# Optimization experiments

Hardware: AMD Instinct MI355X
Metric: run time of the kernel (lower is better)

The kernel has to match this reference:

```python
import jax, jax.numpy as jnp
import numpy as np

I_DIM = 50000
D_DIM = 128
N_EDGES = 800000
N_NODES = I_DIM + 1


def setup_inputs() -> dict:
    key = jax.random.key(0)
    k1, k2, k3, k4 = jax.random.split(key, 4)
    # edge[:,0] must be sorted for the original bincount+repeat normalization to be valid
    src = jnp.sort(jax.random.randint(k1, (N_EDGES,), 0, N_NODES))
    dst = jax.random.randint(k2, (N_EDGES,), 0, N_NODES)
    edge = jnp.stack([src, dst], axis=1).astype(jnp.int64)
    # GlorotNormal-style init for the embedding table and dense layers
    emb_mat = jax.random.normal(k3, (N_NODES, D_DIM), dtype=jnp.float32) * np.sqrt(2.0 / (N_NODES + D_DIM))
    kA, kB = jax.random.split(k4)
    W_scale = jax.random.normal(kA, (D_DIM, D_DIM), dtype=jnp.float32) * np.sqrt(2.0 / (2 * D_DIM))
    b_scale = jnp.zeros((D_DIM,), dtype=jnp.float32)
    W_att = jax.random.normal(kB, (2 * D_DIM, 1), dtype=jnp.float32) * np.sqrt(2.0 / (2 * D_DIM + 1))
    b_att = jnp.zeros((1,), dtype=jnp.float32)
    return {"edge": edge, "emb_mat": emb_mat, "W_scale": W_scale,
            "b_scale": b_scale, "W_att": W_att, "b_att": b_att}


def reference(edge, emb_mat, W_scale, b_scale, W_att, b_att):
    E = edge.shape[0]
    src = edge[:, 0]
    dst = edge[:, 1]
    # gather both endpoints, project: [E, 2, d]
    edge_emb = jnp.einsum('epd,df->epf', emb_mat[edge], W_scale) + b_scale
    edge_emb = edge_emb.reshape(E, -1)                       # [E, 2d]
    att = edge_emb @ W_att + b_att                           # [E, 1]
    att = jnp.where(att >= 0, att, 0.2 * att)                # LeakyReLU(0.2)
    att = jnp.squeeze(att, axis=-1)                          # [E]
    scores = jnp.exp(att - 1.0)
    score_sum = jax.ops.segment_sum(scores, src, num_segments=N_NODES)
    score_norm = scores / score_sum[src]                     # segment softmax
    item_scaled = emb_mat @ W_scale + b_scale                # [N, d]
    msgs = score_norm[:, None] * item_scaled[dst]            # [E, d]
    agg = jax.ops.segment_sum(msgs, src, num_segments=N_NODES)
    return jax.nn.sigmoid(agg)                               # [N, d]
```

## Files before the change

### kernel.cpp

```cpp
#include <hip/hip_runtime.h>
#include <math.h>


#define NN 50001
#define DD 128
#define NE 800000
#define GEMM_BLOCKS 782
#define EDGE_BLOCKS 3125
#define TR_BLOCKS 64

typedef __attribute__((ext_vector_type(8))) short short8;
typedef __attribute__((ext_vector_type(4))) float floatx4;

__device__ __forceinline__ unsigned short f2bf(float f) {
    unsigned u = __builtin_bit_cast(unsigned, f);
    u += 0x7fffu + ((u >> 16) & 1u);
    return (unsigned short)(u >> 16);
}
__device__ __forceinline__ float bflo(unsigned u) {
    return __builtin_bit_cast(float, u << 16);
}
__device__ __forceinline__ float bfhi(unsigned u) {
    return __builtin_bit_cast(float, u & 0xffff0000u);
}
__device__ __forceinline__ float score(float att) {
    att = att >= 0.f ? att : 0.2f * att;
    return __expf(att - 1.f);
}

__global__ void __launch_bounds__(256) k_pre(const float* __restrict__ W,
        const int* __restrict__ edge, unsigned short* __restrict__ WT,
        int* __restrict__ row_ptr) {
    if (blockIdx.x < TR_BLOCKS) {
        int j = blockIdx.x * 2 + (threadIdx.x >> 7);
        int k = threadIdx.x & 127;
        WT[j * DD + k] = f2bf(W[k * DD + j]);
        return;
    }
    int e = (blockIdx.x - TR_BLOCKS) * 256 + threadIdx.x;
    if (e >= NE) return;
    int s = edge[2 * e];
    if (e == 0) {
        for (int n = 0; n <= s; n++) row_ptr[n] = 0;
    } else {
        int p = edge[2 * (e - 1)];
        for (int n = p + 1; n <= s; n++) row_ptr[n] = e;
    }
    if (e == NE - 1) {
        for (int n = s + 1; n <= NN; n++) row_ptr[n] = NE;
    }
}

__global__ void __launch_bounds__(256) k_gemm(const float* __restrict__ emb,
        const unsigned short* __restrict__ WT, const float* __restrict__ b_scale,
        const float* __restrict__ W_att, unsigned short* __restrict__ item,
        float* __restrict__ a_src, float* __restrict__ a_dst,
        const float* __restrict__ b_att) {
    int wave = blockIdx.x * 4 + (threadIdx.x >> 6);
    int lane = threadIdx.x & 63;
    int base = wave * 16;
    if (base >= NN) return;
    int m = lane & 15, q = lane >> 4;
    int node = base + m;
    bool valid = node < NN;

    int row = valid ? node : NN - 1;
    const float* bp = emb + (long)row * DD + q * 8;
    short8 b[4];
    #pragma unroll
    for (int ks = 0; ks < 4; ks++) {
        float4 f0 = *(const float4*)(bp + ks * 32);
        float4 f1 = *(const float4*)(bp + ks * 32 + 4);
        b[ks][0] = (short)f2bf(f0.x); b[ks][1] = (short)f2bf(f0.y);
        b[ks][2] = (short)f2bf(f0.z); b[ks][3] = (short)f2bf(f0.w);
        b[ks][4] = (short)f2bf(f1.x); b[ks][5] = (short)f2bf(f1.y);
        b[ks][6] = (short)f2bf(f1.z); b[ks][7] = (short)f2bf(f1.w);
    }

    float p_src = 0.f, p_dst = 0.f;

    #pragma unroll
    for (int ft = 0; ft < 8; ft++) {
        floatx4 acc = {0.f, 0.f, 0.f, 0.f};
        const unsigned short* wrow = WT + (ft * 16 + m) * DD;
        #pragma unroll
        for (int ks = 0; ks < 4; ks++) {
            short8 a = *(const short8*)(wrow + ks * 32 + q * 8);
            acc = __builtin_amdgcn_mfma_f32_16x16x32_bf16(a, b[ks], acc, 0, 0, 0);
        }
        int fo = ft * 16 + q * 4;
        float4 bs = *(const float4*)(b_scale + fo);
        float4 ws = *(const float4*)(W_att + fo);
        float4 wd = *(const float4*)(W_att + DD + fo);
        float v0 = acc[0] + bs.x, v1 = acc[1] + bs.y;
        float v2 = acc[2] + bs.z, v3 = acc[3] + bs.w;
        if (valid) {
            uint2 pk;
            pk.x = (unsigned)f2bf(v0) | ((unsigned)f2bf(v1) << 16);
            pk.y = (unsigned)f2bf(v2) | ((unsigned)f2bf(v3) << 16);
            *(uint2*)(item + (long)node * DD + fo) = pk;
        }
        p_src += v0 * ws.x + v1 * ws.y + v2 * ws.z + v3 * ws.w;
        p_dst += v0 * wd.x + v1 * wd.y + v2 * wd.z + v3 * wd.w;
    }
    p_src += __shfl_xor(p_src, 16, 64); p_src += __shfl_xor(p_src, 32, 64);
    p_dst += __shfl_xor(p_dst, 16, 64); p_dst += __shfl_xor(p_dst, 32, 64);
    if (q == 0 && valid) { a_src[node] = p_src + b_att[0]; a_dst[node] = p_dst; }
}

#define ACC8(S, U) \
    acc[0] += (S) * bflo((U).x); acc[1] += (S) * bfhi((U).x); \
    acc[2] += (S) * bflo((U).y); acc[3] += (S) * bfhi((U).y); \
    acc[4] += (S) * bflo((U).z); acc[5] += (S) * bfhi((U).z); \
    acc[6] += (S) * bflo((U).w); acc[7] += (S) * bfhi((U).w);

__global__ void __launch_bounds__(256) k_agg(const int* __restrict__ edge,
        const int* __restrict__ row_ptr, const unsigned short* __restrict__ item,
        const float* __restrict__ a_src, const float* __restrict__ a_dst,
        float* __restrict__ out) {
    int n = blockIdx.x * 16 + (threadIdx.x >> 4);
    int t = threadIdx.x & 15;
    if (n >= NN) return;

    int start = row_ptr[n];
    int len = row_ptr[n + 1] - start;
    float* op = out + (long)n * DD + t * 8;

    if (len <= 0) {
        float4 h = make_float4(0.5f, 0.5f, 0.5f, 0.5f);
        *(float4*)op = h;
        *(float4*)(op + 4) = h;
        return;
    }

    float asrc = a_src[n];
    const int* dp = edge + 2 * start + 1;
    const unsigned short* ip = item + t * 8;

    float acc[8] = {0.f, 0.f, 0.f, 0.f, 0.f, 0.f, 0.f, 0.f};
    float ssum = 0.f;

    for (int j = 0; j < len; j += 16) {
        int jj = j + t;
        int idx = jj < len ? jj : len - 1;
        int d = dp[2 * idx];
        float x = a_dst[d];
        float s = (jj < len) ? score(asrc + x) : 0.f;
        ssum += s;

        int cnt = len - j;
        if (cnt > 16) cnt = 16;
        int kk = 0;
        for (; kk + 4 <= cnt; kk += 4) {
            int d0 = __shfl(d, kk, 16),     d1 = __shfl(d, kk + 1, 16);
            int d2 = __shfl(d, kk + 2, 16), d3 = __shfl(d, kk + 3, 16);
            float s0 = __shfl(s, kk, 16),     s1 = __shfl(s, kk + 1, 16);
            float s2 = __shfl(s, kk + 2, 16), s3 = __shfl(s, kk + 3, 16);
            uint4 u0 = *(const uint4*)(ip + (long)d0 * DD);
            uint4 u1 = *(const uint4*)(ip + (long)d1 * DD);
            uint4 u2 = *(const uint4*)(ip + (long)d2 * DD);
            uint4 u3 = *(const uint4*)(ip + (long)d3 * DD);
            ACC8(s0, u0);
            ACC8(s1, u1);
            ACC8(s2, u2);
            ACC8(s3, u3);
        }
        for (; kk < cnt; kk++) {
            int d0 = __shfl(d, kk, 16);
            float s0 = __shfl(s, kk, 16);
            uint4 u0 = *(const uint4*)(ip + (long)d0 * DD);
            ACC8(s0, u0);
        }
    }

    ssum += __shfl_xor(ssum, 1, 16);
    ssum += __shfl_xor(ssum, 2, 16);
    ssum += __shfl_xor(ssum, 4, 16);
    ssum += __shfl_xor(ssum, 8, 16);
    float inv = 1.f / ssum;

    float4 o0, o1;
    o0.x = 1.f / (1.f + __expf(-acc[0] * inv));
    o0.y = 1.f / (1.f + __expf(-acc[1] * inv));
    o0.z = 1.f / (1.f + __expf(-acc[2] * inv));
    o0.w = 1.f / (1.f + __expf(-acc[3] * inv));
    o1.x = 1.f / (1.f + __expf(-acc[4] * inv));
    o1.y = 1.f / (1.f + __expf(-acc[5] * inv));
    o1.z = 1.f / (1.f + __expf(-acc[6] * inv));
    o1.w = 1.f / (1.f + __expf(-acc[7] * inv));
    *(float4*)op = o0;
    *(float4*)(op + 4) = o1;
}

extern "C" void kernel_launch(void* const* d_in, const int* in_sizes, int n_in,
                              void* d_out, int out_size, void* d_ws, size_t ws_size,
                              hipStream_t stream) {
    const int*   edge    = (const int*)d_in[0];
    const float* emb     = (const float*)d_in[1];
    const float* W_scale = (const float*)d_in[2];
    const float* b_scale = (const float*)d_in[3];
    const float* W_att   = (const float*)d_in[4];
    const float* b_att   = (const float*)d_in[5];
    float* out = (float*)d_out;

    char* ws = (char*)d_ws;
    int*            row_ptr = (int*)(ws);
    float*          a_src   = (float*)(ws + 200832);
    float*          a_dst   = (float*)(ws + 401024);
    unsigned short* item    = (unsigned short*)(ws + 601216);
    unsigned short* WT      = (unsigned short*)(ws + 13401472);

    int node_blocks = (NN + 15) / 16;

    k_pre  <<<TR_BLOCKS + EDGE_BLOCKS, 256, 0, stream>>>(W_scale, edge, WT, row_ptr);
    k_gemm <<<GEMM_BLOCKS,             256, 0, stream>>>(emb, WT, b_scale, W_att,
                                                         item, a_src, a_dst, b_att);
    k_agg  <<<node_blocks,             256, 0, stream>>>(edge, row_ptr, item,
                                                         a_src, a_dst, out);
}
```

Before: 143.1 us.

## Apply W_scale after aggregation and fold attention weights into projected vectors

Uses linearity to reorder the work: the attention logits come from emb dotted with W_scale·W_att vectors computed once, and aggregation gathers bf16 raw embeddings, with the W_scale GEMM applied afterwards to the normalized aggregates in a new output kernel. Because the softmax weights sum to one per node, the bias can be added after the projection. This removes the pre-aggregation GEMM from the attention path, but adds a fourth kernel and an intermediate bf16 aggregate round trip, and the rounding points change slightly.

```diff
diff --git a/kernel.cpp b/kernel.cpp
--- a/kernel.cpp
+++ b/kernel.cpp
@@ -5,8 +5,9 @@
 #define NN 50001
 #define DD 128
 #define NE 800000
-#define GEMM_BLOCKS 782
 #define EDGE_BLOCKS 3125
+#define ATT_BLOCKS 3126
+#define OUT_BLOCKS 782
 #define TR_BLOCKS 64
 
 typedef __attribute__((ext_vector_type(8))) short short8;
@@ -29,7 +30,10 @@
 }
 
 __global__ void __launch_bounds__(256) k_pre(const float* __restrict__ W,
-        const int* __restrict__ edge, unsigned short* __restrict__ WT,
+        const float* __restrict__ W_att, const float* __restrict__ b_scale,
+        const float* __restrict__ b_att, const int* __restrict__ edge,
+        unsigned short* __restrict__ WT, float* __restrict__ u_src,
+        float* __restrict__ u_dst, float* __restrict__ cb,
         int* __restrict__ row_ptr) {
     if (blockIdx.x < TR_BLOCKS) {
         int j = blockIdx.x * 2 + (threadIdx.x >> 7);
@@ -37,7 +41,28 @@
         WT[j * DD + k] = f2bf(W[k * DD + j]);
         return;
     }
-    int e = (blockIdx.x - TR_BLOCKS) * 256 + threadIdx.x;
+    if (blockIdx.x == TR_BLOCKS) {
+        int k = threadIdx.x;
+        if (k < DD) {
+            float us = 0.f, ud = 0.f;
+            for (int j = 0; j < DD; j++) {
+                float w = W[k * DD + j];
+                us += w * W_att[j];
+                ud += w * W_att[DD + j];
+            }
+            u_src[k] = us; u_dst[k] = ud;
+        } else if (k == DD) {
+            float c = b_att[0];
+            for (int j = 0; j < DD; j++) c += b_scale[j] * W_att[j];
+            cb[0] = c;
+        } else if (k == DD + 1) {
+            float c = 0.f;
+            for (int j = 0; j < DD; j++) c += b_scale[j] * W_att[DD + j];
+            cb[1] = c;
+        }
+        return;
+    }
+    int e = (blockIdx.x - TR_BLOCKS - 1) * 256 + threadIdx.x;
     if (e >= NE) return;
     int s = edge[2 * e];
     if (e == 0) {
@@ -51,61 +76,39 @@
     }
 }
 
-__global__ void __launch_bounds__(256) k_gemm(const float* __restrict__ emb,
-        const unsigned short* __restrict__ WT, const float* __restrict__ b_scale,
-        const float* __restrict__ W_att, unsigned short* __restrict__ item,
-        float* __restrict__ a_src, float* __restrict__ a_dst,
-        const float* __restrict__ b_att) {
-    int wave = blockIdx.x * 4 + (threadIdx.x >> 6);
-    int lane = threadIdx.x & 63;
-    int base = wave * 16;
-    if (base >= NN) return;
-    int m = lane & 15, q = lane >> 4;
-    int node = base + m;
-    bool valid = node < NN;
-
-    int row = valid ? node : NN - 1;
-    const float* bp = emb + (long)row * DD + q * 8;
-    short8 b[4];
-    #pragma unroll
-    for (int ks = 0; ks < 4; ks++) {
-        float4 f0 = *(const float4*)(bp + ks * 32);
-        float4 f1 = *(const float4*)(bp + ks * 32 + 4);
-        b[ks][0] = (short)f2bf(f0.x); b[ks][1] = (short)f2bf(f0.y);
-        b[ks][2] = (short)f2bf(f0.z); b[ks][3] = (short)f2bf(f0.w);
-        b[ks][4] = (short)f2bf(f1.x); b[ks][5] = (short)f2bf(f1.y);
-        b[ks][6] = (short)f2bf(f1.z); b[ks][7] = (short)f2bf(f1.w);
-    }
-
-    float p_src = 0.f, p_dst = 0.f;
-
-    #pragma unroll
-    for (int ft = 0; ft < 8; ft++) {
-        floatx4 acc = {0.f, 0.f, 0.f, 0.f};
-        const unsigned short* wrow = WT + (ft * 16 + m) * DD;
-        #pragma unroll
-        for (int ks = 0; ks < 4; ks++) {
-            short8 a = *(const short8*)(wrow + ks * 32 + q * 8);
-            acc = __builtin_amdgcn_mfma_f32_16x16x32_bf16(a, b[ks], acc, 0, 0, 0);
-        }
-        int fo = ft * 16 + q * 4;
-        float4 bs = *(const float4*)(b_scale + fo);
-        float4 ws = *(const float4*)(W_att + fo);
-        float4 wd = *(const float4*)(W_att + DD + fo);
-        float v0 = acc[0] + bs.x, v1 = acc[1] + bs.y;
-        float v2 = acc[2] + bs.z, v3 = acc[3] + bs.w;
-        if (valid) {
-            uint2 pk;
-            pk.x = (unsigned)f2bf(v0) | ((unsigned)f2bf(v1) << 16);
-            pk.y = (unsigned)f2bf(v2) | ((unsigned)f2bf(v3) << 16);
-            *(uint2*)(item + (long)node * DD + fo) = pk;
-        }
-        p_src += v0 * ws.x + v1 * ws.y + v2 * ws.z + v3 * ws.w;
-        p_dst += v0 * wd.x + v1 * wd.y + v2 * wd.z + v3 * wd.w;
-    }
-    p_src += __shfl_xor(p_src, 16, 64); p_src += __shfl_xor(p_src, 32, 64);
-    p_dst += __shfl_xor(p_dst, 16, 64); p_dst += __shfl_xor(p_dst, 32, 64);
-    if (q == 0 && valid) { a_src[node] = p_src + b_att[0]; a_dst[node] = p_dst; }
+__global__ void __launch_bounds__(256) k_att(const float* __restrict__ emb,
+        const float* __restrict__ u_src, const float* __restrict__ u_dst,
+        const float* __restrict__ cb, unsigned short* __restrict__ emb_bf,
+        float* __restrict__ a_src, float* __restrict__ a_dst) {
+    int n = blockIdx.x * 16 + (threadIdx.x >> 4);
+    int t = threadIdx.x & 15;
+    if (n >= NN) return;
+
+    const float* ep = emb + (long)n * DD + t * 8;
+    float4 e0 = *(const float4*)(ep);
+    float4 e1 = *(const float4*)(ep + 4);
+    float4 us0 = *(const float4*)(u_src + t * 8);
+    float4 us1 = *(const float4*)(u_src + t * 8 + 4);
+    float4 ud0 = *(const float4*)(u_dst + t * 8);
+    float4 ud1 = *(const float4*)(u_dst + t * 8 + 4);
+
+    float ps = e0.x * us0.x + e0.y * us0.y + e0.z * us0.z + e0.w * us0.w
+             + e1.x * us1.x + e1.y * us1.y + e1.z * us1.z + e1.w * us1.w;
+    float pd = e0.x * ud0.x + e0.y * ud0.y + e0.z * ud0.z + e0.w * ud0.w
+             + e1.x * ud1.x + e1.y * ud1.y + e1.z * ud1.z + e1.w * ud1.w;
+
+    uint4 pk;
+    pk.x = (unsigned)f2bf(e0.x) | ((unsigned)f2bf(e0.y) << 16);
+    pk.y = (unsigned)f2bf(e0.z) | ((unsigned)f2bf(e0.w) << 16);
+    pk.z = (unsigned)f2bf(e1.x) | ((unsigned)f2bf(e1.y) << 16);
+    pk.w = (unsigned)f2bf(e1.z) | ((unsigned)f2bf(e1.w) << 16);
+    *(uint4*)(emb_bf + (long)n * DD + t * 8) = pk;
+
+    ps += __shfl_xor(ps, 1, 16); ps += __shfl_xor(ps, 2, 16);
+    ps += __shfl_xor(ps, 4, 16); ps += __shfl_xor(ps, 8, 16);
+    pd += __shfl_xor(pd, 1, 16); pd += __shfl_xor(pd, 2, 16);
+    pd += __shfl_xor(pd, 4, 16); pd += __shfl_xor(pd, 8, 16);
+    if (t == 0) { a_src[n] = ps + cb[0]; a_dst[n] = pd + cb[1]; }
 }
 
 #define ACC8(S, U) \
@@ -115,27 +118,26 @@
     acc[6] += (S) * bflo((U).w); acc[7] += (S) * bfhi((U).w);
 
 __global__ void __launch_bounds__(256) k_agg(const int* __restrict__ edge,
-        const int* __restrict__ row_ptr, const unsigned short* __restrict__ item,
+        const int* __restrict__ row_ptr, const unsigned short* __restrict__ emb_bf,
         const float* __restrict__ a_src, const float* __restrict__ a_dst,
-        float* __restrict__ out) {
+        unsigned short* __restrict__ aggN) {
     int n = blockIdx.x * 16 + (threadIdx.x >> 4);
     int t = threadIdx.x & 15;
     if (n >= NN) return;
 
     int start = row_ptr[n];
     int len = row_ptr[n + 1] - start;
-    float* op = out + (long)n * DD + t * 8;
+    unsigned short* op = aggN + (long)n * DD + t * 8;
 
     if (len <= 0) {
-        float4 h = make_float4(0.5f, 0.5f, 0.5f, 0.5f);
-        *(float4*)op = h;
-        *(float4*)(op + 4) = h;
+        uint4 z = make_uint4(0u, 0u, 0u, 0u);
+        *(uint4*)op = z;
         return;
     }
 
     float asrc = a_src[n];
     const int* dp = edge + 2 * start + 1;
-    const unsigned short* ip = item + t * 8;
+    const unsigned short* ip = emb_bf + t * 8;
 
     float acc[8] = {0.f, 0.f, 0.f, 0.f, 0.f, 0.f, 0.f, 0.f};
     float ssum = 0.f;
@@ -179,17 +181,57 @@
     ssum += __shfl_xor(ssum, 8, 16);
     float inv = 1.f / ssum;
 
-    float4 o0, o1;
-    o0.x = 1.f / (1.f + __expf(-acc[0] * inv));
-    o0.y = 1.f / (1.f + __expf(-acc[1] * inv));
-    o0.z = 1.f / (1.f + __expf(-acc[2] * inv));
-    o0.w = 1.f / (1.f + __expf(-acc[3] * inv));
-    o1.x = 1.f / (1.f + __expf(-acc[4] * inv));
-    o1.y = 1.f / (1.f + __expf(-acc[5] * inv));
-    o1.z = 1.f / (1.f + __expf(-acc[6] * inv));
-    o1.w = 1.f / (1.f + __expf(-acc[7] * inv));
-    *(float4*)op = o0;
-    *(float4*)(op + 4) = o1;
+    uint4 pk;
+    pk.x = (unsigned)f2bf(acc[0] * inv) | ((unsigned)f2bf(acc[1] * inv) << 16);
+    pk.y = (unsigned)f2bf(acc[2] * inv) | ((unsigned)f2bf(acc[3] * inv) << 16);
+    pk.z = (unsigned)f2bf(acc[4] * inv) | ((unsigned)f2bf(acc[5] * inv) << 16);
+    pk.w = (unsigned)f2bf(acc[6] * inv) | ((unsigned)f2bf(acc[7] * inv) << 16);
+    *(uint4*)op = pk;
+}
+
+__global__ void __launch_bounds__(256) k_out(const unsigned short* __restrict__ aggN,
+        const unsigned short* __restrict__ WT, const float* __restrict__ b_scale,
+        const int* __restrict__ row_ptr, float* __restrict__ out) {
+    int wave = blockIdx.x * 4 + (threadIdx.x >> 6);
+    int lane = threadIdx.x & 63;
+    int base = wave * 16;
+    if (base >= NN) return;
+    int m = lane & 15, q = lane >> 4;
+    int node = base + m;
+    bool valid = node < NN;
+    int row = valid ? node : NN - 1;
+    int len = row_ptr[row + 1] - row_ptr[row];
+
+    const unsigned short* bp = aggN + (long)row * DD + q * 8;
+    short8 b[4];
+    #pragma unroll
+    for (int ks = 0; ks < 4; ks++)
+        b[ks] = *(const short8*)(bp + ks * 32);
+
+    #pragma unroll
+    for (int ft = 0; ft < 8; ft++) {
+        floatx4 acc = {0.f, 0.f, 0.f, 0.f};
+        const unsigned short* wrow = WT + (ft * 16 + m) * DD + q * 8;
+        #pragma unroll
+        for (int ks = 0; ks < 4; ks++) {
+            short8 a = *(const short8*)(wrow + ks * 32);
+            acc = __builtin_amdgcn_mfma_f32_16x16x32_bf16(a, b[ks], acc, 0, 0, 0);
+        }
+        if (valid) {
+            int fo = ft * 16 + q * 4;
+            float4 bs = *(const float4*)(b_scale + fo);
+            float4 o;
+            if (len > 0) {
+                o.x = 1.f / (1.f + __expf(-(acc[0] + bs.x)));
+                o.y = 1.f / (1.f + __expf(-(acc[1] + bs.y)));
+                o.z = 1.f / (1.f + __expf(-(acc[2] + bs.z)));
+                o.w = 1.f / (1.f + __expf(-(acc[3] + bs.w)));
+            } else {
+                o = make_float4(0.5f, 0.5f, 0.5f, 0.5f);
+            }
+            *(float4*)(out + (long)node * DD + fo) = o;
+        }
+    }
 }
 
 extern "C" void kernel_launch(void* const* d_in, const int* in_sizes, int n_in,
@@ -207,14 +249,19 @@
     int*            row_ptr = (int*)(ws);
     float*          a_src   = (float*)(ws + 200832);
     float*          a_dst   = (float*)(ws + 401024);
-    unsigned short* item    = (unsigned short*)(ws + 601216);
-    unsigned short* WT      = (unsigned short*)(ws + 13401472);
-
-    int node_blocks = (NN + 15) / 16;
-
-    k_pre  <<<TR_BLOCKS + EDGE_BLOCKS, 256, 0, stream>>>(W_scale, edge, WT, row_ptr);
-    k_gemm <<<GEMM_BLOCKS,             256, 0, stream>>>(emb, WT, b_scale, W_att,
-                                                         item, a_src, a_dst, b_att);
-    k_agg  <<<node_blocks,             256, 0, stream>>>(edge, row_ptr, item,
-                                                         a_src, a_dst, out);
-}
+    unsigned short* emb_bf  = (unsigned short*)(ws + 601216);
+    unsigned short* aggN    = (unsigned short*)(ws + 13401472);
+    unsigned short* WT      = (unsigned short*)(ws + 26201728);
+    float*          u_src   = (float*)(ws + 26234496);
+    float*          u_dst   = (float*)(ws + 26235008);
+    float*          cb      = (float*)(ws + 26235520);
+
+    k_pre <<<TR_BLOCKS + 1 + EDGE_BLOCKS, 256, 0, stream>>>(W_scale, W_att, b_scale,
+                                                            b_att, edge, WT, u_src,
+                                                            u_dst, cb, row_ptr);
+    k_att <<<ATT_BLOCKS,  256, 0, stream>>>(emb, u_src, u_dst, cb, emb_bf,
+                                            a_src, a_dst);
+    k_agg <<<ATT_BLOCKS,  256, 0, stream>>>(edge, row_ptr, emb_bf, a_src, a_dst,
+                                            aggN);
+    k_out <<<OUT_BLOCKS,  256, 0, stream>>>(aggN, WT, b_scale, row_ptr, out);
+}
```

New measurement: 145.6 us. About the same (+1.7%).
